# Optimization experiments

Hardware: AMD Instinct MI355X
Metric: run time of the kernel (lower is better)

Reference implementation:

```python
import jax, jax.numpy as jnp
import numpy as np

B, S, E, H = 4, 2048, 768, 12
D = E // H  # head dimension = 64


def setup_inputs() -> dict:
    key = jax.random.key(0)
    ks = jax.random.split(key, 10)
    scale = 1.0 / np.sqrt(E)
    x = jax.random.normal(ks[0], (B, S, E), dtype=jnp.float32)
    mask = jax.random.randint(ks[1], (B, S), 0, 2, dtype=jnp.int32)
    # per-head Q/K/V projections stacked over heads: [H, E, D]
    Wq = jax.random.normal(ks[2], (H, E, D), dtype=jnp.float32) * scale
    bq = jax.random.normal(ks[3], (H, D), dtype=jnp.float32) * scale
    Wk = jax.random.normal(ks[4], (H, E, D), dtype=jnp.float32) * scale
    bk = jax.random.normal(ks[5], (H, D), dtype=jnp.float32) * scale
    Wv = jax.random.normal(ks[6], (H, E, D), dtype=jnp.float32) * scale
    bv = jax.random.normal(ks[7], (H, D), dtype=jnp.float32) * scale
    # output projection: [H*D, E]
    Wo = jax.random.normal(ks[8], (H * D, E), dtype=jnp.float32) * scale
    bo = jax.random.normal(ks[9], (E,), dtype=jnp.float32) * scale
    return {"x": x, "mask": mask, "Wq": Wq, "bq": bq, "Wk": Wk, "bk": bk,
            "Wv": Wv, "bv": bv, "Wo": Wo, "bo": bo}


def reference(x, mask, Wq, bq, Wk, bk, Wv, bv, Wo, bo):
    # Per-head linear projections, vectorized over heads: [B, H, S, D]
    q = jnp.einsum('bse,hed->bhsd', x, Wq) + bq[None, :, None, :]
    k = jnp.einsum('bse,hed->bhsd', x, Wk) + bk[None, :, None, :]
    v = jnp.einsum('bse,hed->bhsd', x, Wv) + bv[None, :, None, :]
    # scores: [B, H, S, S]
    scores = jnp.einsum('bhqd,bhkd->bhqk', q, k) / jnp.sqrt(jnp.float32(D))
    # mask [B, S] broadcast over heads and query positions (key-side mask)
    key_mask = mask[:, None, None, :]  # [B, 1, 1, S]
    scores = jnp.where(key_mask == 0, jnp.float32(-1e9), scores)
    attn = jax.nn.softmax(scores, axis=-1)
    out = jnp.einsum('bhqk,bhkd->bhqd', attn, v)  # [B, H, S, D]
    # concat heads: [B, S, H*D]
    out = out.transpose(0, 2, 1, 3).reshape(B, S, H * D)
    return out @ Wo + bo
```

## Files before the change

### kernel.cpp

```cpp
#include <hip/hip_runtime.h>
#include <hip/hip_bf16.h>

#define B_ 4
#define S_ 2048
#define E_ 768
#define H_ 12
#define D_ 64
#define M_ (B_*S_)
#define NQKV 2304
#define KDIM 768

typedef __bf16 bf16x8 __attribute__((ext_vector_type(8)));
typedef float f32x4 __attribute__((ext_vector_type(4)));
typedef short shortx4 __attribute__((ext_vector_type(4)));
typedef unsigned int uintx2 __attribute__((ext_vector_type(2)));
typedef unsigned int uintx4 __attribute__((ext_vector_type(4)));

typedef __attribute__((address_space(1))) void gvoid;
typedef __attribute__((address_space(3))) void lvoid;

__device__ __forceinline__ void gl_lds16(const void* g, void* l) {
  __builtin_amdgcn_global_load_lds((gvoid*)g, (lvoid*)l, 16, 0, 0);
}

__device__ __forceinline__ f32x4 mfma16(bf16x8 a, bf16x8 b, f32x4 c) {
  return __builtin_amdgcn_mfma_f32_16x16x32_bf16(a, b, c, 0, 0, 0);
}

__device__ __forceinline__ f32x4 mfma_pv(shortx4 a, shortx4 b, f32x4 c) {
#if __has_builtin(__builtin_amdgcn_mfma_f32_16x16x16bf16_1k)
  return __builtin_amdgcn_mfma_f32_16x16x16bf16_1k(a, b, c, 0, 0, 0);
#else
  uintx2 au = __builtin_bit_cast(uintx2, a);
  uintx2 bu = __builtin_bit_cast(uintx2, b);
  uintx4 aw = {au.x, au.y, 0u, 0u};
  uintx4 bw = {bu.x, bu.y, 0u, 0u};
  return mfma16(__builtin_bit_cast(bf16x8, aw), __builtin_bit_cast(bf16x8, bw), c);
#endif
}

__device__ __forceinline__ __bf16 ldmix(const void* p, size_t idx, int is_bf) {
  if (is_bf) return ((const __bf16*)p)[idx];
  return (__bf16)(((const float*)p)[idx]);
}
__device__ __forceinline__ float ldmixf(const void* p, size_t idx, int is_bf) {
  if (is_bf) return (float)((const __bf16*)p)[idx];
  return ((const float*)p)[idx];
}

__global__ __launch_bounds__(256) void prep_kernel(
    const void* __restrict__ x, const int* __restrict__ mask,
    const void* __restrict__ Wq, const void* __restrict__ bq,
    const void* __restrict__ Wk, const void* __restrict__ bk,
    const void* __restrict__ Wv, const void* __restrict__ bv,
    const void* __restrict__ Wo, const void* __restrict__ bo,
    int* __restrict__ flag,
    __bf16* __restrict__ Xb,
    __bf16* __restrict__ WbT, __bf16* __restrict__ WoT,
    float* __restrict__ biasP, float* __restrict__ biasO,
    int* __restrict__ R, int* __restrict__ npadArr, int* __restrict__ narrArr)
{
  const int t = threadIdx.x;
  const int bid = blockIdx.x;

  if (bid < 4) {
    __shared__ int wtot[4];
    __shared__ int runningS;
    const int w = t >> 6, lane = t & 63;
    const int b = bid;
    if (t == 0) runningS = 0;
    __syncthreads();
    for (int k0 = 0; k0 < S_; k0 += 256) {
      int keep = (mask[b * S_ + k0 + t] != 0) ? 1 : 0;
      unsigned long long bal = __ballot(keep);
      int lanePre = __popcll(bal & ((1ull << lane) - 1ull));
      if (lane == 0) wtot[w] = __popcll(bal);
      __syncthreads();
      int base = runningS;
      for (int i = 0; i < w; ++i) base += wtot[i];
      if (keep) R[b * S_ + base + lanePre] = b * S_ + k0 + t;
      __syncthreads();
      if (t == 0) runningS += wtot[0] + wtot[1] + wtot[2] + wtot[3];
      __syncthreads();
    }
    int n = runningS;
    for (int j = n + t; j < S_; j += 256)
      R[b * S_ + j] = b * S_;
    if (t == 0) { npadArr[b] = (n + 63) & ~63; narrArr[b] = n; }
    return;
  }

  __shared__ int scnt[4];
  {
    const unsigned short* xr = (const unsigned short*)x;
    unsigned short h = xr[2 * t];
    int e = (h >> 7) & 0xFF;
    unsigned long long bal = __ballot(e >= 100 && e <= 140);
    if ((t & 63) == 0) scnt[t >> 6] = __popcll(bal);
  }
  __syncthreads();
  const int is_bf = (scnt[0] + scnt[1] + scnt[2] + scnt[3] > 148) ? 1 : 0;
  if (bid == 4 && t == 0) *flag = is_bf;

  const int cb = bid - 4;
  if (cb < 3072) {
    int base = (cb * 256 + t) * 8;
    if (is_bf) {
      *(uintx4*)(Xb + base) = *(const uintx4*)((const __bf16*)x + base);
    } else {
      const float* xf = (const float*)x + base;
      f32x4 a = *(const f32x4*)xf;
      f32x4 c = *(const f32x4*)(xf + 4);
      __bf16 ov[8] = {(__bf16)a[0], (__bf16)a[1], (__bf16)a[2], (__bf16)a[3],
                      (__bf16)c[0], (__bf16)c[1], (__bf16)c[2], (__bf16)c[3]};
      *(uintx4*)(Xb + base) = *(uintx4*)ov;
    }
    return;
  }
  int idx = (cb - 3072) * 256 + t;
  const int NW = NQKV * KDIM;
  if (idx < NW) {
    int n = idx / KDIM;
    int e = idx - n * KDIM;
    int sel = n / 768;
    int hd  = n - sel * 768;
    int h = hd >> 6, d = hd & 63;
    const void* W = (sel == 0) ? Wq : (sel == 1) ? Wk : Wv;
    WbT[idx] = ldmix(W, (size_t)(h * 768 + e) * 64 + d, is_bf);
  } else {
    int idx2 = idx - NW;
    int n = idx2 / 768;
    int k = idx2 - n * 768;
    WoT[idx2] = ldmix(Wo, (size_t)k * 768 + n, is_bf);
  }
  if (idx < NQKV) {
    int sel = idx / 768;
    int hd = idx - sel * 768;
    const void* bsel = (sel == 0) ? bq : (sel == 1) ? bk : bv;
    biasP[idx] = ldmixf(bsel, hd, is_bf);
  }
  if (idx >= NW && idx < NW + 768) {
    biasO[idx - NW] = ldmixf(bo, idx - NW, is_bf);
  }
}

__global__ __launch_bounds__(256) void gemm_qkv(
    const __bf16* __restrict__ Xb,
    const __bf16* __restrict__ WbT,
    const float* __restrict__ biasP,
    const int* __restrict__ R,
    const int* __restrict__ npadArr,
    __bf16* __restrict__ Qc,
    __bf16* __restrict__ Kc,
    __bf16* __restrict__ Vc)
{
  __shared__ __align__(16) __bf16 As[128 * 32];
  __shared__ __align__(16) __bf16 Bs[128 * 32];
  const int t = threadIdx.x;
  const int wave = t >> 6, lane = t & 63;
  const int l15 = lane & 15, lq = lane >> 4;
  const int wm = (wave & 1) * 64;
  const int wn = (wave >> 1) * 64;

  const int bid = blockIdx.x;
  int m0, bn0, isQ, b = 0;
  int rowA0, rowA1;
  if (bid < 384) {
    isQ = 1;
    int mi = bid / 6, ni = bid - mi * 6;
    m0 = mi * 128; bn0 = ni * 128;
    rowA0 = m0 + (t >> 2);
    rowA1 = m0 + 64 + (t >> 2);
  } else {
    isQ = 0;
    int r2 = bid - 384;
    b = r2 / 192;
    int rr = r2 - b * 192;
    int mi = rr / 12, ni = rr - mi * 12;
    int np = npadArr[b];
    np = (np < 0) ? 0 : ((np > 2048) ? 2048 : np);
    if (mi * 128 >= np) return;
    m0 = mi * 128;
    bn0 = 768 + ni * 128;
    rowA0 = R[b * S_ + m0 + (t >> 2)] & (M_ - 1);
    rowA1 = R[b * S_ + m0 + 64 + (t >> 2)] & (M_ - 1);
  }
  const int c8 = (t & 3) << 3;
  const int brow0 = bn0 + (t >> 2);
  const int brow1 = bn0 + 64 + (t >> 2);

  const f32x4 z4 = {0.f, 0.f, 0.f, 0.f};
  f32x4 acc[4][4];
#pragma unroll
  for (int i = 0; i < 4; ++i)
#pragma unroll
    for (int j = 0; j < 4; ++j) acc[i][j] = z4;

  for (int k0 = 0; k0 < KDIM; k0 += 32) {
    __syncthreads();
    gl_lds16(Xb + (size_t)rowA0 * KDIM + k0 + c8, As + (size_t)wave * 512);
    gl_lds16(Xb + (size_t)rowA1 * KDIM + k0 + c8, As + (size_t)(2048 + wave * 512));
    gl_lds16(WbT + (size_t)brow0 * KDIM + k0 + c8, Bs + (size_t)wave * 512);
    gl_lds16(WbT + (size_t)brow1 * KDIM + k0 + c8, Bs + (size_t)(2048 + wave * 512));
    __syncthreads();
    bf16x8 af[4], bfr[4];
#pragma unroll
    for (int i = 0; i < 4; ++i) af[i]  = *(const bf16x8*)(As + (wm + i * 16 + l15) * 32 + lq * 8);
#pragma unroll
    for (int j = 0; j < 4; ++j) bfr[j] = *(const bf16x8*)(Bs + (wn + j * 16 + l15) * 32 + lq * 8);
#pragma unroll
    for (int i = 0; i < 4; ++i)
#pragma unroll
      for (int j = 0; j < 4; ++j)
        acc[i][j] = mfma16(af[i], bfr[j], acc[i][j]);
  }

#pragma unroll
  for (int j = 0; j < 4; ++j) {
    if (isQ) {
      int nn = bn0 + wn + j * 16 + l15;
      float bv = biasP[nn];
#pragma unroll
      for (int i = 0; i < 4; ++i) {
        int mbase = m0 + wm + i * 16 + lq * 4;
#pragma unroll
        for (int r = 0; r < 4; ++r)
          Qc[(size_t)(mbase + r) * 768 + nn] = (__bf16)(acc[i][j][r] + bv);
      }
    } else {
      int nn = (bn0 - 768) + wn + j * 16 + l15;
      float bv = biasP[768 + nn];
      const int isK = (nn < 768);
      const int hh = (isK ? nn : nn - 768) >> 6;
      const int d  = nn & 63;
      const size_t bhh = (size_t)(b * H_ + hh);
#pragma unroll
      for (int i = 0; i < 4; ++i) {
        int jbase = m0 + wm + i * 16 + lq * 4;
#pragma unroll
        for (int r = 0; r < 4; ++r) {
          int jj = jbase + r;
          __bf16 ov = (__bf16)(acc[i][j][r] + bv);
          if (isK) Kc[(bhh * 2048 + jj) * 64 + d] = ov;
          else     Vc[(bhh * 512 + (jj >> 2)) * 256 + d * 4 + (jj & 3)] = ov;
        }
      }
    }
  }
}

__global__ __launch_bounds__(256) void gemm_out(
    const __bf16* __restrict__ A,
    const __bf16* __restrict__ WoT,
    const float* __restrict__ biasO,
    void* __restrict__ C,
    const int* __restrict__ flag)
{
  __shared__ __align__(16) __bf16 As[128 * 32];
  __shared__ __align__(16) __bf16 Bs[128 * 32];
  const int obf = *flag;
  const int t = threadIdx.x;
  const int wave = t >> 6, lane = t & 63;
  const int l15 = lane & 15, lq = lane >> 4;
  const int wm = (wave & 1) * 64;
  const int wn = (wave >> 1) * 64;
  const int m0 = blockIdx.x * 128;
  const int n0 = blockIdx.y * 128;
  const int c8 = (t & 3) << 3;
  const int rowA0 = m0 + (t >> 2);
  const int rowA1 = m0 + 64 + (t >> 2);
  const int brow0 = n0 + (t >> 2);
  const int brow1 = n0 + 64 + (t >> 2);

  const f32x4 z4 = {0.f, 0.f, 0.f, 0.f};
  f32x4 acc[4][4];
#pragma unroll
  for (int i = 0; i < 4; ++i)
#pragma unroll
    for (int j = 0; j < 4; ++j) acc[i][j] = z4;

  for (int k0 = 0; k0 < KDIM; k0 += 32) {
    __syncthreads();
    gl_lds16(A + (size_t)rowA0 * KDIM + k0 + c8, As + (size_t)wave * 512);
    gl_lds16(A + (size_t)rowA1 * KDIM + k0 + c8, As + (size_t)(2048 + wave * 512));
    gl_lds16(WoT + (size_t)brow0 * KDIM + k0 + c8, Bs + (size_t)wave * 512);
    gl_lds16(WoT + (size_t)brow1 * KDIM + k0 + c8, Bs + (size_t)(2048 + wave * 512));
    __syncthreads();
    bf16x8 af[4], bfr[4];
#pragma unroll
    for (int i = 0; i < 4; ++i) af[i]  = *(const bf16x8*)(As + (wm + i * 16 + l15) * 32 + lq * 8);
#pragma unroll
    for (int j = 0; j < 4; ++j) bfr[j] = *(const bf16x8*)(Bs + (wn + j * 16 + l15) * 32 + lq * 8);
#pragma unroll
    for (int i = 0; i < 4; ++i)
#pragma unroll
      for (int j = 0; j < 4; ++j)
        acc[i][j] = mfma16(af[i], bfr[j], acc[i][j]);
  }

#pragma unroll
  for (int j = 0; j < 4; ++j) {
    int n = n0 + wn + j * 16 + l15;
    float bv = biasO[n];
#pragma unroll
    for (int i = 0; i < 4; ++i) {
      int mbase = m0 + wm + i * 16 + lq * 4;
#pragma unroll
      for (int r = 0; r < 4; ++r) {
        size_t off = (size_t)(mbase + r) * 768 + n;
        float val = acc[i][j][r] + bv;
        if (obf) ((__bf16*)C)[off] = (__bf16)val;
        else     ((float*)C)[off]  = val;
      }
    }
  }
}

__global__ __launch_bounds__(256) void attn_kernel(
    const __bf16* __restrict__ Qc,
    const __bf16* __restrict__ Kc,
    const __bf16* __restrict__ Vc,
    const int* __restrict__ npadArr,
    const int* __restrict__ narrArr,
    __bf16* __restrict__ Out)
{
  __shared__ __align__(16) __bf16 Ks0[2][64 * 32];
  __shared__ __align__(16) __bf16 Ks1[2][64 * 32];
  __shared__ __align__(16) __bf16 Vt[2][16 * 256];

  const int t = threadIdx.x;
  const int w = t >> 6, lane = t & 63;
  const int l15 = lane & 15, qd = lane >> 4;
  const int bh = blockIdx.y;
  const int b = bh / H_, h = bh - b * H_;
  const int q0 = blockIdx.x * 64;
  int Skv = npadArr[b];
  Skv = (Skv < 0) ? 0 : ((Skv > 2048) ? 2048 : Skv);
  int nb = narrArr[b];
  nb = (nb < 0) ? 0 : ((nb > Skv) ? Skv : nb);

  const __bf16* Qb = Qc + (size_t)b * S_ * E_ + h * 64;
  const __bf16* Kb = Kc + (size_t)bh * 2048 * 64;
  const __bf16* Vg = Vc + (size_t)bh * 512 * 256;

  bf16x8 qf[2];
  {
    int qrow = q0 + w * 16 + l15;
    qf[0] = *(const bf16x8*)(Qb + (size_t)qrow * E_ + qd * 8);
    qf[1] = *(const bf16x8*)(Qb + (size_t)qrow * E_ + 32 + qd * 8);
  }

  const f32x4 z4 = {0.f, 0.f, 0.f, 0.f};
  f32x4 o[4];
#pragma unroll
  for (int dt = 0; dt < 4; ++dt) o[dt] = z4;
  f32x4 ol = z4;

  const short one_bf = (short)0x3F80;
  const shortx4 ones4 = {one_bf, one_bf, one_bf, one_bf};

  const int skey = t >> 2;
  const int sch  = (((t & 3) ^ ((t >> 3) & 3)) * 8);
  const int qsw  = ((qd ^ ((l15 >> 1) & 3)) * 8);
  const float SC = 0.18033688011112042f;

  const int nt = Skv >> 6;
  if (nt > 0) {
    gl_lds16(Kb + (size_t)skey * 64 + sch,      &Ks0[0][w * 512]);
    gl_lds16(Kb + (size_t)skey * 64 + 32 + sch, &Ks1[0][w * 512]);
    gl_lds16(Vg + t * 8,        &Vt[0][w * 512]);
    gl_lds16(Vg + 2048 + t * 8, &Vt[0][2048 + w * 512]);
  }

  for (int ti = 0; ti < nt; ++ti) {
    const int k0 = ti << 6;
    const int cur = ti & 1;
    if (ti + 1 < nt) {
      const int nxt = cur ^ 1;
      const int kk = k0 + 64;
      gl_lds16(Kb + (size_t)(kk + skey) * 64 + sch,      &Ks0[nxt][w * 512]);
      gl_lds16(Kb + (size_t)(kk + skey) * 64 + 32 + sch, &Ks1[nxt][w * 512]);
      const __bf16* vsrc = Vg + ((size_t)(kk >> 2)) * 256;
      gl_lds16(vsrc + t * 8,        &Vt[nxt][w * 512]);
      gl_lds16(vsrc + 2048 + t * 8, &Vt[nxt][2048 + w * 512]);
      asm volatile("s_waitcnt vmcnt(4)" ::: "memory");
    } else {
      asm volatile("s_waitcnt vmcnt(0)" ::: "memory");
    }
    __builtin_amdgcn_s_barrier();

    const __bf16* K0 = Ks0[cur];
    const __bf16* K1 = Ks1[cur];
    const __bf16* Vb = Vt[cur];

    bf16x8 kf[4][2];
#pragma unroll
    for (int kt = 0; kt < 4; ++kt) {
      kf[kt][0] = *(const bf16x8*)(K0 + (kt * 16 + l15) * 32 + qsw);
      kf[kt][1] = *(const bf16x8*)(K1 + (kt * 16 + l15) * 32 + qsw);
    }
    shortx4 vf[4][4];
#pragma unroll
    for (int kt = 0; kt < 4; ++kt)
#pragma unroll
      for (int dt = 0; dt < 4; ++dt)
        vf[kt][dt] = *(const shortx4*)(Vb + (kt * 4 + qd) * 256 + (dt * 16 + l15) * 4);

    f32x4 ma[4];
    if (k0 + 64 <= nb) {
#pragma unroll
      for (int kt = 0; kt < 4; ++kt) ma[kt] = z4;
    } else {
#pragma unroll
      for (int kt = 0; kt < 4; ++kt) {
        int kk = k0 + kt * 16 + qd * 4;
#pragma unroll
        for (int r = 0; r < 4; ++r)
          ma[kt][r] = (kk + r < nb) ? 0.f : -1.0e9f;
      }
    }

    {
      f32x4 s[4];
#pragma unroll
      for (int kt = 0; kt < 4; ++kt) {
        s[kt] = mfma16(kf[kt][0], qf[0], z4);
        s[kt] = mfma16(kf[kt][1], qf[1], s[kt]);
      }
      shortx4 pfr[4];
#pragma unroll
      for (int kt = 0; kt < 4; ++kt) {
        float p0 = __builtin_amdgcn_exp2f(__builtin_fmaf(s[kt][0], SC, ma[kt][0]));
        float p1 = __builtin_amdgcn_exp2f(__builtin_fmaf(s[kt][1], SC, ma[kt][1]));
        float p2 = __builtin_amdgcn_exp2f(__builtin_fmaf(s[kt][2], SC, ma[kt][2]));
        float p3 = __builtin_amdgcn_exp2f(__builtin_fmaf(s[kt][3], SC, ma[kt][3]));
        unsigned int lo16 = __builtin_amdgcn_perm(__builtin_bit_cast(unsigned int, p1),
                                                  __builtin_bit_cast(unsigned int, p0), 0x07060302u);
        unsigned int hi16 = __builtin_amdgcn_perm(__builtin_bit_cast(unsigned int, p3),
                                                  __builtin_bit_cast(unsigned int, p2), 0x07060302u);
        uintx2 u = {lo16, hi16};
        pfr[kt] = __builtin_bit_cast(shortx4, u);
      }
#pragma unroll
      for (int dt = 0; dt < 4; ++dt)
#pragma unroll
        for (int kt = 0; kt < 4; ++kt)
          o[dt] = mfma_pv(pfr[kt], vf[kt][dt], o[dt]);
#pragma unroll
      for (int kt = 0; kt < 4; ++kt)
        ol = mfma_pv(pfr[kt], ones4, ol);
    }

    __builtin_amdgcn_s_barrier();
  }

#pragma unroll
  for (int dt = 0; dt < 4; ++dt)
#pragma unroll
    for (int r = 0; r < 4; ++r) {
      int qrow = q0 + w * 16 + qd * 4 + r;
      Out[(size_t)(b * S_ + qrow) * E_ + h * 64 + dt * 16 + l15] =
          (__bf16)(o[dt][r] / ol[r]);
    }
}

extern "C" void kernel_launch(void* const* d_in, const int* in_sizes, int n_in,
                              void* d_out, int out_size, void* d_ws, size_t ws_size,
                              hipStream_t stream) {
  const void* x  = d_in[0];
  const int* mask = (const int*)d_in[1];
  const void* Wq = d_in[2];
  const void* bq = d_in[3];
  const void* Wk = d_in[4];
  const void* bk = d_in[5];
  const void* Wv = d_in[6];
  const void* bv = d_in[7];
  const void* Wo = d_in[8];
  const void* bo = d_in[9];

  char* ws = (char*)d_ws;
  int*    flag  = (int*)(ws + 0);
  __bf16* Xb    = (__bf16*)(ws + 256);
  __bf16* WbT   = (__bf16*)(ws + 12583168);
  __bf16* WoT   = (__bf16*)(ws + 16122112);
  float*  biasP = (float*)(ws + 17301760);
  float*  biasO = (float*)(ws + 17310976);
  __bf16* Qc    = (__bf16*)(ws + 17314048);
  __bf16* Kc    = (__bf16*)(ws + 29896960);
  __bf16* Vc    = (__bf16*)(ws + 42479872);
  __bf16* attnO = (__bf16*)(ws + 55062784);
  int*    Ridx  = (int*)(ws + 67645696);
  int*    npad  = (int*)(ws + 67711232);
  int*    narr  = (int*)(ws + 67711248);

  prep_kernel<<<dim3(12292), dim3(256), 0, stream>>>(
      x, mask, Wq, bq, Wk, bk, Wv, bv, Wo, bo,
      flag, Xb, WbT, WoT, biasP, biasO, Ridx, npad, narr);
  gemm_qkv<<<dim3(1152), dim3(256), 0, stream>>>(Xb, WbT, biasP, Ridx, npad, Qc, Kc, Vc);
  attn_kernel<<<dim3(32, 48), dim3(256), 0, stream>>>(Qc, Kc, Vc, npad, narr, attnO);
  gemm_out<<<dim3(64, 6), dim3(256), 0, stream>>>(attnO, WoT, biasO, d_out, flag);
}
```

Baseline: 216.6 us.

## Drop LDS double buffering; read V fragments directly from global memory

The attention loop no longer double-buffers K and V in LDS with asynchronous prefetch. K is staged into a single LDS buffer each iteration, guarded by two block barriers, and V fragments are loaded straight from global memory into registers. LDS use per block falls from about 32 KB to 8 KB, which may allow more resident blocks per CU to hide latency. The cost is that loads are no longer overlapped with compute inside a block, and the V reads become uncoalesced global traffic.

```diff
diff --git a/kernel.cpp b/kernel.cpp
--- a/kernel.cpp
+++ b/kernel.cpp
@@ -324,9 +324,8 @@
     const int* __restrict__ narrArr,
     __bf16* __restrict__ Out)
 {
-  __shared__ __align__(16) __bf16 Ks0[2][64 * 32];
-  __shared__ __align__(16) __bf16 Ks1[2][64 * 32];
-  __shared__ __align__(16) __bf16 Vt[2][16 * 256];
+  __shared__ __align__(16) __bf16 Ks0[64 * 32];
+  __shared__ __align__(16) __bf16 Ks1[64 * 32];
 
   const int t = threadIdx.x;
   const int w = t >> 6, lane = t & 63;
@@ -365,46 +364,21 @@
   const float SC = 0.18033688011112042f;
 
   const int nt = Skv >> 6;
-  if (nt > 0) {
-    gl_lds16(Kb + (size_t)skey * 64 + sch,      &Ks0[0][w * 512]);
-    gl_lds16(Kb + (size_t)skey * 64 + 32 + sch, &Ks1[0][w * 512]);
-    gl_lds16(Vg + t * 8,        &Vt[0][w * 512]);
-    gl_lds16(Vg + 2048 + t * 8, &Vt[0][2048 + w * 512]);
-  }
-
   for (int ti = 0; ti < nt; ++ti) {
     const int k0 = ti << 6;
-    const int cur = ti & 1;
-    if (ti + 1 < nt) {
-      const int nxt = cur ^ 1;
-      const int kk = k0 + 64;
-      gl_lds16(Kb + (size_t)(kk + skey) * 64 + sch,      &Ks0[nxt][w * 512]);
-      gl_lds16(Kb + (size_t)(kk + skey) * 64 + 32 + sch, &Ks1[nxt][w * 512]);
-      const __bf16* vsrc = Vg + ((size_t)(kk >> 2)) * 256;
-      gl_lds16(vsrc + t * 8,        &Vt[nxt][w * 512]);
-      gl_lds16(vsrc + 2048 + t * 8, &Vt[nxt][2048 + w * 512]);
-      asm volatile("s_waitcnt vmcnt(4)" ::: "memory");
-    } else {
-      asm volatile("s_waitcnt vmcnt(0)" ::: "memory");
-    }
-    __builtin_amdgcn_s_barrier();
-
-    const __bf16* K0 = Ks0[cur];
-    const __bf16* K1 = Ks1[cur];
-    const __bf16* Vb = Vt[cur];
-
-    bf16x8 kf[4][2];
-#pragma unroll
-    for (int kt = 0; kt < 4; ++kt) {
-      kf[kt][0] = *(const bf16x8*)(K0 + (kt * 16 + l15) * 32 + qsw);
-      kf[kt][1] = *(const bf16x8*)(K1 + (kt * 16 + l15) * 32 + qsw);
-    }
+    __syncthreads();
+    gl_lds16(Kb + (size_t)(k0 + skey) * 64 + sch,      Ks0 + w * 512);
+    gl_lds16(Kb + (size_t)(k0 + skey) * 64 + 32 + sch, Ks1 + w * 512);
+
     shortx4 vf[4][4];
-#pragma unroll
-    for (int kt = 0; kt < 4; ++kt)
-#pragma unroll
-      for (int dt = 0; dt < 4; ++dt)
-        vf[kt][dt] = *(const shortx4*)(Vb + (kt * 4 + qd) * 256 + (dt * 16 + l15) * 4);
+    {
+      const __bf16* vt0 = Vg + (size_t)(ti * 16) * 256 + qd * 256 + (size_t)l15 * 4;
+#pragma unroll
+      for (int kt = 0; kt < 4; ++kt)
+#pragma unroll
+        for (int dt = 0; dt < 4; ++dt)
+          vf[kt][dt] = *(const shortx4*)(vt0 + kt * 1024 + dt * 64);
+    }
 
     f32x4 ma[4];
     if (k0 + 64 <= nb) {
@@ -418,6 +392,15 @@
         for (int r = 0; r < 4; ++r)
           ma[kt][r] = (kk + r < nb) ? 0.f : -1.0e9f;
       }
+    }
+
+    __syncthreads();
+
+    bf16x8 kf[4][2];
+#pragma unroll
+    for (int kt = 0; kt < 4; ++kt) {
+      kf[kt][0] = *(const bf16x8*)(Ks0 + (kt * 16 + l15) * 32 + qsw);
+      kf[kt][1] = *(const bf16x8*)(Ks1 + (kt * 16 + l15) * 32 + qsw);
     }
 
     {
@@ -450,8 +433,6 @@
       for (int kt = 0; kt < 4; ++kt)
         ol = mfma_pv(pfr[kt], ones4, ol);
     }
-
-    __builtin_amdgcn_s_barrier();
   }
 
 #pragma unroll
```

New measurement: 230.6 us. 1.06x slower.
